# Kernel tuning notes

Measured on AMD Instinct MI355X. Metric: run time of the kernel, lower is better.

## Reference

```python
import jax, jax.numpy as jnp
import numpy as np

N_NODES = 500000
N_EDGES = 600000
N_GRAPHS = 4096
X_DIM = 128
H_DIM = 128
Z_DIM = 64
BN_EPS = 1e-5


def setup_inputs() -> dict:
    key = jax.random.key(0)
    ks = jax.random.split(key, 16)
    inp = {
        'x': jax.random.normal(ks[0], (N_NODES, X_DIM), dtype=jnp.float32),
        'edge_index': jax.random.randint(ks[1], (2, N_EDGES), 0, N_NODES),
        'edge_weights': jax.random.uniform(ks[2], (N_EDGES,), dtype=jnp.float32),
        'y_target': jax.random.uniform(ks[3], (N_GRAPHS, 1), dtype=jnp.float32),
        'batch': jnp.sort(jax.random.randint(ks[4], (N_NODES,), 0, N_GRAPHS)),
        # embedder (single weighted GCN-style layer) params
        'W_self': jax.random.normal(ks[5], (X_DIM, H_DIM), dtype=jnp.float32) / np.sqrt(X_DIM),
        'W_nbr': jax.random.normal(ks[6], (X_DIM, H_DIM), dtype=jnp.float32) / np.sqrt(X_DIM),
        'b_emb': jnp.zeros((H_DIM,), dtype=jnp.float32),
        # encoder_mean head: Linear(h_dim+1, z_dim) + BatchNorm1d(z_dim) + ReLU
        'W_mu': jax.random.normal(ks[7], (H_DIM + 1, Z_DIM), dtype=jnp.float32) / np.sqrt(H_DIM + 1),
        'b_mu': jnp.zeros((Z_DIM,), dtype=jnp.float32),
        'gamma_mu': jnp.ones((Z_DIM,), dtype=jnp.float32),
        'beta_mu': jnp.zeros((Z_DIM,), dtype=jnp.float32),
        # encoder_var head: Linear + BN + ReLU + Sigmoid
        'W_var': jax.random.normal(ks[8], (H_DIM + 1, Z_DIM), dtype=jnp.float32) / np.sqrt(H_DIM + 1),
        'b_var': jnp.zeros((Z_DIM,), dtype=jnp.float32),
        'gamma_var': jnp.ones((Z_DIM,), dtype=jnp.float32),
        'beta_var': jnp.zeros((Z_DIM,), dtype=jnp.float32),
    }
    return inp


def _batchnorm(a, gamma, beta):
    # BatchNorm1d in training mode: per-feature batch stats (biased var)
    mu = jnp.mean(a, axis=0, keepdims=True)
    var = jnp.mean((a - mu) ** 2, axis=0, keepdims=True)
    return (a - mu) * jax.lax.rsqrt(var + BN_EPS) * gamma + beta


def reference(x, edge_index, edge_weights, y_target, batch,
              W_self, W_nbr, b_emb,
              W_mu, b_mu, gamma_mu, beta_mu,
              W_var, b_var, gamma_var, beta_var):
    src, dst = edge_index[0], edge_index[1]
    # embedder.embedding(x, edge_index, edge_weights): weighted neighbor agg + self
    msg = jax.ops.segment_sum(edge_weights[:, None] * x[src], dst, num_segments=N_NODES)
    embed = jax.nn.relu(x @ W_self + msg @ W_nbr + b_emb)  # [N, H]
    # global_mean_pool over graph ids
    sums = jax.ops.segment_sum(embed, batch, num_segments=N_GRAPHS)      # [G, H]
    counts = jax.ops.segment_sum(jnp.ones((embed.shape[0],), embed.dtype), batch,
                                 num_segments=N_GRAPHS)
    graph_emb = sums / jnp.maximum(counts, 1.0)[:, None]
    # concat y_target -> [G, H+1]
    h = jnp.concatenate([graph_emb, y_target], axis=1)
    z_mu = jax.nn.relu(_batchnorm(h @ W_mu + b_mu, gamma_mu, beta_mu))
    z_logvar = jax.nn.sigmoid(jax.nn.relu(_batchnorm(h @ W_var + b_var, gamma_var, beta_var)))
    return (z_mu, z_logvar)
```

## Files before the change

kernel.cpp:

```cpp
#include <hip/hip_runtime.h>
#include <hip/hip_bf16.h>
#include <stdint.h>

#define N_NODES 500000
#define N_EDGES 600000
#define N_GRAPHS 4096
#define XD 128
#define HD 128
#define ZD 64
#define BROWS 64
#define NBUCKETS 7813
#define CAP 120

#define OFF_CURS   0ull
#define OFF_SUMS   8192ull
#define OFF_DEG    532480ull
#define OFF_NINFO  1032704ull
#define OFF_CURSOR 1532928ull
#define OFF_SBUF   2033152ull
#define OFF_AT     3909120ull
#define OFF_STATS  4433408ull
#define OFF_WT     4433664ull
#define OFF_GMEAN  4450048ull
#define OFF_PART   4974336ull
#define OFF_PAY    12974848ull

typedef __attribute__((ext_vector_type(8))) short bf16x8;
typedef __attribute__((ext_vector_type(4))) float f32x4;

__device__ inline uint32_t pk_bf16(float lo, float hi) {
  uint32_t ul = __float_as_uint(lo); ul += 0x7fffu + ((ul >> 16) & 1u);
  uint32_t uh = __float_as_uint(hi); uh += 0x7fffu + ((uh >> 16) & 1u);
  return (ul >> 16) | (uh & 0xffff0000u);
}
__device__ inline float bl16(uint32_t u) { return __uint_as_float(u << 16); }
__device__ inline float bh16(uint32_t u) { return __uint_as_float(u & 0xffff0000u); }

__global__ void wprep_kernel(const float* __restrict__ Wnbr, const float* __restrict__ Wself,
                             uint32_t* __restrict__ wt) {
  const float* __restrict__ W = blockIdx.x ? Wself : Wnbr;
  uint32_t* __restrict__ out = wt + (size_t)blockIdx.x * 8192;
  const int t = threadIdx.x;
  const int n = t >> 1, h = t & 1;
  for (int q = 0; q < 32; ++q) {
    int k2 = h * 32 + q;
    float lo = W[(2 * k2) * HD + n];
    float hi = W[(2 * k2 + 1) * HD + n];
    out[n * 64 + k2] = pk_bf16(lo, hi);
  }
}

__global__ void deg_count(const int* __restrict__ ei, uint32_t* __restrict__ deg) {
  int e = blockIdx.x * blockDim.x + threadIdx.x;
  if (e >= N_EDGES) return;
  atomicAdd(deg + ei[N_EDGES + e], 1u);
}

__global__ void scan_prefix(const uint32_t* __restrict__ deg, uint32_t* __restrict__ nodeinfo,
                            uint32_t* __restrict__ cursor) {
  const int b = blockIdx.x;
  const int lane = threadIdx.x;
  int n = b * BROWS + lane;
  int d = (n < N_NODES) ? (int)deg[n] : 0;
  int s = d;
#pragma unroll
  for (int off = 1; off < 64; off <<= 1) {
    int t = __shfl_up(s, off, 64);
    if (lane >= off) s += t;
  }
  int excl = s - d;
  int st = excl < CAP ? excl : CAP;
  int en = (excl + d) < CAP ? (excl + d) : CAP;
  if (n < N_NODES) {
    nodeinfo[n] = (uint32_t)st | ((uint32_t)en << 8);
    cursor[n] = 0u;
  }
}

__global__ void bucket_fill(const int* __restrict__ ei, const float* __restrict__ ew,
                            const uint32_t* __restrict__ nodeinfo, uint32_t* __restrict__ cursor,
                            int* __restrict__ cur_s, uint2* __restrict__ sbuf,
                            uint32_t* __restrict__ payload) {
  int e = blockIdx.x * blockDim.x + threadIdx.x;
  if (e >= N_EDGES) return;
  int src = ei[e];
  int dst = ei[N_EDGES + e];
  float w = ew[e];
  uint32_t info = nodeinfo[dst];
  int st = (int)(info & 0xffu), en = (int)((info >> 8) & 0xffu);
  int slot = (int)atomicAdd(cursor + dst, 1u);
  int pin = st + slot;
  if (pin >= en) return;
  uint32_t pos = (uint32_t)((dst >> 6) * CAP + pin);
  int bs = src >> 6;
  int ss = atomicAdd(cur_s + bs, 1);
  if (ss < CAP) {
    sbuf[(size_t)bs * CAP + ss] =
        make_uint2(((uint32_t)(src & 63) << 20) | pos, __float_as_uint(w));
  } else {
    uint4 z = make_uint4(0, 0, 0, 0);
    uint4* p = (uint4*)((char*)payload + (size_t)pos * 256);
#pragma unroll
    for (int i = 0; i < 16; ++i) p[i] = z;
  }
}

__launch_bounds__(512, 4)
__global__ void gemm_scatter(const float* __restrict__ x, const uint32_t* __restrict__ wt,
                             const uint2* __restrict__ sbuf, const int* __restrict__ cur_s,
                             uint32_t* __restrict__ payload) {
  __shared__ char lb[33728];
  uint2* srec = (uint2*)(lb + 32768);
  const int b = blockIdx.x;
  const int tid = threadIdx.x;
  const int node0 = b * BROWS;
  const int l = tid & 63, w = tid >> 6;
  const int wm = w >> 2, wn = w & 3;
  const int lr = l & 15, lk = l >> 4;

  {
    const int row = tid >> 3, c8 = tid & 7;
    int m = node0 + row;
    int mc = m < N_NODES ? m : N_NODES - 1;
    const float* xr = x + (size_t)mc * XD + c8 * 16;
    uint32_t p[8];
#pragma unroll
    for (int i = 0; i < 4; ++i) {
      float4 t4 = *(const float4*)(xr + i * 4);
      p[2 * i]     = pk_bf16(t4.x, t4.y);
      p[2 * i + 1] = pk_bf16(t4.z, t4.w);
    }
    char* aw = lb + row * 256;
    const int s0 = c8 * 2;
    *(uint4*)(aw + (((s0)     ^ (row & 7)) << 4)) = make_uint4(p[0], p[1], p[2], p[3]);
    *(uint4*)(aw + (((s0 + 1) ^ (row & 7)) << 4)) = make_uint4(p[4], p[5], p[6], p[7]);
  }
  if (tid < CAP) srec[tid] = sbuf[(size_t)b * CAP + tid];
  __syncthreads();

  f32x4 acc0[2][2];
#pragma unroll
  for (int mf = 0; mf < 2; ++mf) { acc0[mf][0] = (f32x4)0.f; acc0[mf][1] = (f32x4)0.f; }

  {
    const char* wtb = (const char*)wt;
#pragma unroll
    for (int kb = 0; kb < 4; ++kb) {
      int slot = (kb << 2) | lk;
      bf16x8 bf0 = *(const bf16x8*)(wtb + (wn * 32 + lr) * 256 + (kb << 6) + (lk << 4));
      bf16x8 bf1 = *(const bf16x8*)(wtb + (wn * 32 + 16 + lr) * 256 + (kb << 6) + (lk << 4));
#pragma unroll
      for (int mf = 0; mf < 2; ++mf) {
        int r = wm * 32 + mf * 16 + lr;
        bf16x8 a = *(const bf16x8*)(lb + r * 256 + ((slot ^ (r & 7)) << 4));
        acc0[mf][0] = __builtin_amdgcn_mfma_f32_16x16x32_bf16(a, bf0, acc0[mf][0], 0, 0, 0);
        acc0[mf][1] = __builtin_amdgcn_mfma_f32_16x16x32_bf16(a, bf1, acc0[mf][1], 0, 0, 0);
      }
    }
  }
  __syncthreads();

  {
#pragma unroll
    for (int mf = 0; mf < 2; ++mf)
#pragma unroll
      for (int nf = 0; nf < 2; ++nf) {
        int col = wn * 32 + nf * 16 + lr;
#pragma unroll
        for (int r = 0; r < 4; ++r) {
          int row = wm * 32 + mf * 16 + lk * 4 + r;
          uint32_t uv = __float_as_uint(acc0[mf][nf][r]);
          uv += 0x7fffu + ((uv >> 16) & 1u);
          *(unsigned short*)(lb + 16384 + row * 256 + ((col * 2) ^ ((row & 7) << 4))) =
              (unsigned short)(uv >> 16);
        }
      }
  }
  __syncthreads();

  {
    int cnt = cur_s[b]; if (cnt > CAP) cnt = CAP;
    const int eg = tid >> 5;
    const int c = tid & 31;
#pragma unroll
    for (int k = 0; k < 8; ++k) {
      int s = eg + (k << 4);
      if (s < cnt) {
        uint2 rec = srec[s];
        int srcloc = (int)(rec.x >> 20);
        uint32_t pos = rec.x & 0xFFFFFu;
        float wgt = __uint_as_float(rec.y);
        uint2 uv = *(const uint2*)(lb + 16384 + srcloc * 256 + ((c * 8) ^ ((srcloc & 7) << 4)));
        float a0 = bl16(uv.x) * wgt, a1 = bh16(uv.x) * wgt;
        float a2 = bl16(uv.y) * wgt, a3 = bh16(uv.y) * wgt;
        *(uint2*)((char*)payload + (size_t)pos * 256 + c * 8) =
            make_uint2(pk_bf16(a0, a1), pk_bf16(a2, a3));
      }
    }
  }
}

__launch_bounds__(512, 4)
__global__ void accum_pool(const float* __restrict__ x, const uint32_t* __restrict__ payload,
                           const uint32_t* __restrict__ nodeinfo,
                           const uint32_t* __restrict__ wt, const float* __restrict__ bemb,
                           const int* __restrict__ batch,
                           float* __restrict__ partials, float* __restrict__ sums) {
  __shared__ float lds[5200];
  char* astage = (char*)lds;
  float* P = lds + 4096;
  int* span = (int*)(lds + 5120);
  const int b = blockIdx.x;
  const int tid = threadIdx.x;
  const int node0 = b * BROWS;
  const int gfirst = batch[node0];
  const int grp = tid >> 5, c = tid & 31;
  const int l = tid & 63, w = tid >> 6;
  const int wm = w >> 2, wn = w & 3;
  const int lr = l & 15, lk = l >> 4;

  for (int i = tid; i < 1024; i += 512) P[i] = 0.f;
  if (tid < 64) {
    int m = node0 + tid;
    span[tid] = (m < N_NODES) ? (batch[m] - gfirst) : -1;
  }

  {
    const int row = tid >> 3, c8 = tid & 7;
    int m = node0 + row;
    int mc = m < N_NODES ? m : N_NODES - 1;
    const float* xr = x + (size_t)mc * XD + c8 * 16;
    uint32_t p[8];
#pragma unroll
    for (int i = 0; i < 4; ++i) {
      float4 t4 = *(const float4*)(xr + i * 4);
      p[2 * i]     = pk_bf16(t4.x, t4.y);
      p[2 * i + 1] = pk_bf16(t4.z, t4.w);
    }
    char* aw = astage + row * 256;
    const int s0 = c8 * 2;
    *(uint4*)(aw + (((s0)     ^ (row & 7)) << 4)) = make_uint4(p[0], p[1], p[2], p[3]);
    *(uint4*)(aw + (((s0 + 1) ^ (row & 7)) << 4)) = make_uint4(p[4], p[5], p[6], p[7]);
  }
  __syncthreads();

  f32x4 acc1[2][2];
#pragma unroll
  for (int mf = 0; mf < 2; ++mf) { acc1[mf][0] = (f32x4)0.f; acc1[mf][1] = (f32x4)0.f; }
  {
    const char* wtb = (const char*)wt + 32768;
#pragma unroll
    for (int kb = 0; kb < 4; ++kb) {
      int slot = (kb << 2) | lk;
      bf16x8 bf0 = *(const bf16x8*)(wtb + (wn * 32 + lr) * 256 + (kb << 6) + (lk << 4));
      bf16x8 bf1 = *(const bf16x8*)(wtb + (wn * 32 + 16 + lr) * 256 + (kb << 6) + (lk << 4));
#pragma unroll
      for (int mf = 0; mf < 2; ++mf) {
        int r = wm * 32 + mf * 16 + lr;
        bf16x8 a = *(const bf16x8*)(astage + r * 256 + ((slot ^ (r & 7)) << 4));
        acc1[mf][0] = __builtin_amdgcn_mfma_f32_16x16x32_bf16(a, bf0, acc1[mf][0], 0, 0, 0);
        acc1[mf][1] = __builtin_amdgcn_mfma_f32_16x16x32_bf16(a, bf1, acc1[mf][1], 0, 0, 0);
      }
    }
  }
  __syncthreads();

  {
    float be0 = bemb[wn * 32 + lr];
    float be1 = bemb[wn * 32 + 16 + lr];
#pragma unroll
    for (int mf = 0; mf < 2; ++mf)
#pragma unroll
      for (int nf = 0; nf < 2; ++nf) {
        int col = wn * 32 + nf * 16 + lr;
        float be = nf ? be1 : be0;
#pragma unroll
        for (int r = 0; r < 4; ++r) {
          int row = wm * 32 + mf * 16 + lk * 4 + r;
          uint32_t uv = __float_as_uint(acc1[mf][nf][r] + be);
          uv += 0x7fffu + ((uv >> 16) & 1u);
          *(unsigned short*)(astage + row * 256 + ((col * 2) ^ ((row & 7) << 4))) =
              (unsigned short)(uv >> 16);
        }
      }
  }
  __syncthreads();

  {
    float p0 = 0.f, p1 = 0.f, p2 = 0.f, p3 = 0.f;
    int jcur = -1;
#pragma unroll
    for (int rr = 0; rr < 4; ++rr) {
      int row = grp * 4 + rr;
      int n = node0 + row;
      int j = span[row];
      float a0 = 0.f, a1 = 0.f, a2 = 0.f, a3 = 0.f;
      uint32_t info = (n < N_NODES) ? nodeinfo[n] : 0u;
      int st = (int)(info & 0xffu), en = (int)((info >> 8) & 0xffu);
      for (int i = st; i < en; ++i) {
        uint2 pv = *(const uint2*)(payload + ((size_t)b * CAP + i) * 64 + (c << 1));
        a0 += bl16(pv.x); a1 += bh16(pv.x);
        a2 += bl16(pv.y); a3 += bh16(pv.y);
      }
      if (j >= 0) {
        uint2 vv = *(const uint2*)(astage + row * 256 + ((c * 8) ^ ((row & 7) << 4)));
        float z0 = fmaxf(a0 + bl16(vv.x), 0.f);
        float z1 = fmaxf(a1 + bh16(vv.x), 0.f);
        float z2 = fmaxf(a2 + bl16(vv.y), 0.f);
        float z3 = fmaxf(a3 + bh16(vv.y), 0.f);
        if (j != jcur) {
          if (jcur >= 0) {
            if (jcur < 8) {
              atomicAdd(&P[jcur * 128 + 4 * c + 0], p0);
              atomicAdd(&P[jcur * 128 + 4 * c + 1], p1);
              atomicAdd(&P[jcur * 128 + 4 * c + 2], p2);
              atomicAdd(&P[jcur * 128 + 4 * c + 3], p3);
            } else {
              float* sp = sums + (size_t)(gfirst + jcur) * HD + 4 * c;
              atomicAdd(sp + 0, p0); atomicAdd(sp + 1, p1);
              atomicAdd(sp + 2, p2); atomicAdd(sp + 3, p3);
            }
          }
          p0 = p1 = p2 = p3 = 0.f; jcur = j;
        }
        p0 += z0; p1 += z1; p2 += z2; p3 += z3;
      }
    }
    if (jcur >= 0) {
      if (jcur < 8) {
        atomicAdd(&P[jcur * 128 + 4 * c + 0], p0);
        atomicAdd(&P[jcur * 128 + 4 * c + 1], p1);
        atomicAdd(&P[jcur * 128 + 4 * c + 2], p2);
        atomicAdd(&P[jcur * 128 + 4 * c + 3], p3);
      } else {
        float* sp = sums + (size_t)(gfirst + jcur) * HD + 4 * c;
        atomicAdd(sp + 0, p0); atomicAdd(sp + 1, p1);
        atomicAdd(sp + 2, p2); atomicAdd(sp + 3, p3);
      }
    }
  }
  __syncthreads();

  {
    float2 v = *(float2*)&P[tid * 2];
    *(float2*)(partials + (size_t)b * 1024 + tid * 2) = v;
  }
}

__global__ void reduce_mean(const float* __restrict__ partials, const float* __restrict__ sums,
                            const int* __restrict__ batch, float* __restrict__ gmean) {
  const int g = blockIdx.x;
  const int t = threadIdx.x;
  int lo = 0, hi = N_NODES;
  while (lo < hi) { int mid = (lo + hi) >> 1; if (batch[mid] < g) lo = mid + 1; else hi = mid; }
  int s = lo; hi = N_NODES;
  while (lo < hi) { int mid = (lo + hi) >> 1; if (batch[mid] < g + 1) lo = mid + 1; else hi = mid; }
  int e = lo;
  float tot = sums[(size_t)g * HD + t];
  int cnt = e - s;
  if (cnt > 0) {
    int b0 = s >> 6, b1 = (e - 1) >> 6;
    for (int b = b0; b <= b1; ++b) {
      int j = g - batch[b * 64];
      if (j >= 0 && j < 8) tot += partials[(size_t)b * 1024 + j * 128 + t];
    }
  }
  gmean[(size_t)g * HD + t] = tot / fmaxf((float)cnt, 1.f);
}

__global__ void head_kernel(const float* __restrict__ gmean, const float* __restrict__ y,
                            const float* __restrict__ Wmu, const float* __restrict__ bmu,
                            const float* __restrict__ Wvar, const float* __restrict__ bvar,
                            float* __restrict__ aT) {
  __shared__ float hrow[129];
  const int g = blockIdx.x;
  const int t = threadIdx.x;
  hrow[t] = gmean[(size_t)g * HD + t];
  if (t == 0) hrow[128] = y[g];
  __syncthreads();
  const int head = t >> 6, n = t & 63;
  const float* __restrict__ W = head ? Wvar : Wmu;
  float acc = head ? bvar[n] : bmu[n];
  for (int k = 0; k < 129; ++k) acc = fmaf(hrow[k], W[k * ZD + n], acc);
  aT[(size_t)(head * ZD + n) * N_GRAPHS + g] = acc;
}

__global__ void bnstats_kernel(const float* __restrict__ aT, float* __restrict__ stats) {
  const int f = blockIdx.x;
  const float* base = aT + (size_t)f * N_GRAPHS;
  float s = 0.f, ss = 0.f;
  for (int i = threadIdx.x; i < N_GRAPHS; i += 256) { float v = base[i]; s += v; ss += v * v; }
#pragma unroll
  for (int off = 1; off < 64; off <<= 1) { s += __shfl_xor(s, off, 64); ss += __shfl_xor(ss, off, 64); }
  __shared__ float ls[8];
  const int wav = threadIdx.x >> 6, lane = threadIdx.x & 63;
  if (lane == 0) { ls[wav * 2] = s; ls[wav * 2 + 1] = ss; }
  __syncthreads();
  if (threadIdx.x == 0) {
    float S = ls[0] + ls[2] + ls[4] + ls[6];
    float SS = ls[1] + ls[3] + ls[5] + ls[7];
    float mean = S / (float)N_GRAPHS;
    float var = SS / (float)N_GRAPHS - mean * mean;
    stats[f * 2] = mean;
    stats[f * 2 + 1] = rsqrtf(var + 1e-5f);
  }
}

__global__ void bnapply_kernel(const float* __restrict__ aT, const float* __restrict__ stats,
                               const float* __restrict__ gm, const float* __restrict__ btm,
                               const float* __restrict__ gv, const float* __restrict__ btv,
                               float* __restrict__ out) {
  int t = blockIdx.x * blockDim.x + threadIdx.x;
  if (t >= 2 * N_GRAPHS * ZD) return;
  int head = t >> 18;
  int r = t & (N_GRAPHS * ZD - 1);
  int g = r >> 6, n = r & 63;
  int f = (head << 6) | n;
  float v = aT[(size_t)f * N_GRAPHS + g];
  float z = (v - stats[f * 2]) * stats[f * 2 + 1];
  z = z * (head ? gv[n] : gm[n]) + (head ? btv[n] : btm[n]);
  z = fmaxf(z, 0.f);
  if (head) z = 1.f / (1.f + __expf(-z));
  out[t] = z;
}

extern "C" void kernel_launch(void* const* d_in, const int* in_sizes, int n_in,
                              void* d_out, int out_size, void* d_ws, size_t ws_size,
                              hipStream_t stream) {
  const float* x      = (const float*)d_in[0];
  const int*   ei     = (const int*)d_in[1];
  const float* ew     = (const float*)d_in[2];
  const float* y      = (const float*)d_in[3];
  const int*   batch  = (const int*)d_in[4];
  const float* Wself  = (const float*)d_in[5];
  const float* Wnbr   = (const float*)d_in[6];
  const float* bemb   = (const float*)d_in[7];
  const float* Wmu    = (const float*)d_in[8];
  const float* bmu    = (const float*)d_in[9];
  const float* gmu    = (const float*)d_in[10];
  const float* betamu = (const float*)d_in[11];
  const float* Wvar   = (const float*)d_in[12];
  const float* bvar   = (const float*)d_in[13];
  const float* gvar   = (const float*)d_in[14];
  const float* betavar= (const float*)d_in[15];

  float* ws         = (float*)d_ws;
  int*   cur_s      = (int*)(ws + OFF_CURS);
  float* sums       = ws + OFF_SUMS;
  uint32_t* deg     = (uint32_t*)(ws + OFF_DEG);
  uint32_t* ninfo   = (uint32_t*)(ws + OFF_NINFO);
  uint32_t* cursor  = (uint32_t*)(ws + OFF_CURSOR);
  uint2* sbuf       = (uint2*)(ws + OFF_SBUF);
  float* aT         = ws + OFF_AT;
  float* stats      = ws + OFF_STATS;
  uint32_t* wt      = (uint32_t*)(ws + OFF_WT);
  float* gmean      = ws + OFF_GMEAN;
  float* partials   = ws + OFF_PART;
  uint32_t* payload = (uint32_t*)(ws + OFF_PAY);

  hipMemsetAsync(ws, 0, (8192ull + 524288ull + 500224ull) * 4ull, stream);

  wprep_kernel<<<2, 256, 0, stream>>>(Wnbr, Wself, wt);
  deg_count<<<(N_EDGES + 255) / 256, 256, 0, stream>>>(ei, deg);
  scan_prefix<<<NBUCKETS, 64, 0, stream>>>(deg, ninfo, cursor);
  bucket_fill<<<(N_EDGES + 255) / 256, 256, 0, stream>>>(ei, ew, ninfo, cursor,
                                                         cur_s, sbuf, payload);
  gemm_scatter<<<NBUCKETS, 512, 0, stream>>>(x, wt, sbuf, cur_s, payload);
  accum_pool<<<NBUCKETS, 512, 0, stream>>>(x, payload, ninfo, wt, bemb, batch,
                                           partials, sums);
  reduce_mean<<<N_GRAPHS, 128, 0, stream>>>(partials, sums, batch, gmean);
  head_kernel<<<N_GRAPHS, 128, 0, stream>>>(gmean, y, Wmu, bmu, Wvar, bvar, aT);
  bnstats_kernel<<<128, 256, 0, stream>>>(aT, stats);
  bnapply_kernel<<<(2 * N_GRAPHS * ZD + 255) / 256, 256, 0, stream>>>(
      aT, stats, gmu, betamu, gvar, betavar, (float*)d_out);
}
```

Measured before the change: 432.6 us.

## Compute self-GEMM in gemm_scatter, store bf16 V to global, lean pooling kernel

Moves the x@W_self + bias MFMA product out of the pooling kernel and into gemm_scatter, which already has x staged in LDS. The result is written to a new global bf16 buffer, so x is read once instead of twice. The pooling kernel now only gathers the payload and V, uses less LDS, and has a higher occupancy bound. The payload layout also changes from a fixed CAP slot per bucket to a compact prefix-summed layout, built by a new single-block bucket scan. This removes the per-bucket cap on incoming edges, but adds a 128 MB bf16 intermediate round trip and a serial scan launch.

```diff
diff --git a/kernel.cpp b/kernel.cpp
--- a/kernel.cpp
+++ b/kernel.cpp
@@ -17,13 +17,16 @@
 #define OFF_DEG    532480ull
 #define OFF_NINFO  1032704ull
 #define OFF_CURSOR 1532928ull
-#define OFF_SBUF   2033152ull
-#define OFF_AT     3909120ull
-#define OFF_STATS  4433408ull
-#define OFF_WT     4433664ull
-#define OFF_GMEAN  4450048ull
-#define OFF_PART   4974336ull
-#define OFF_PAY    12974848ull
+#define OFF_BTOT   2033152ull
+#define OFF_BBASE  2041344ull
+#define OFF_SBUF   2049536ull
+#define OFF_AT     3925504ull
+#define OFF_STATS  4449792ull
+#define OFF_WT     4450048ull
+#define OFF_GMEAN  4466432ull
+#define OFF_PART   4990720ull
+#define OFF_V      12991232ull
+#define OFF_PAY    44991232ull
 
 typedef __attribute__((ext_vector_type(8))) short bf16x8;
 typedef __attribute__((ext_vector_type(4))) float f32x4;
@@ -57,7 +60,7 @@
 }
 
 __global__ void scan_prefix(const uint32_t* __restrict__ deg, uint32_t* __restrict__ nodeinfo,
-                            uint32_t* __restrict__ cursor) {
+                            uint32_t* __restrict__ cursor, uint32_t* __restrict__ btot) {
   const int b = blockIdx.x;
   const int lane = threadIdx.x;
   int n = b * BROWS + lane;
@@ -69,16 +72,45 @@
     if (lane >= off) s += t;
   }
   int excl = s - d;
-  int st = excl < CAP ? excl : CAP;
-  int en = (excl + d) < CAP ? (excl + d) : CAP;
+  int ex = excl < 255 ? excl : 255;
+  int dc = d < 255 ? d : 255;
   if (n < N_NODES) {
-    nodeinfo[n] = (uint32_t)st | ((uint32_t)en << 8);
+    nodeinfo[n] = (uint32_t)ex | ((uint32_t)dc << 8);
     cursor[n] = 0u;
   }
+  if (lane == 63) btot[b] = (uint32_t)s;
+}
+
+__global__ void scan_buckets(const uint32_t* __restrict__ btot, uint32_t* __restrict__ bbase) {
+  __shared__ uint32_t carry;
+  __shared__ uint32_t wsum[8];
+  if (threadIdx.x == 0) carry = 0u;
+  __syncthreads();
+  for (int off = 0; off < NBUCKETS; off += 512) {
+    int i = off + (int)threadIdx.x;
+    uint32_t d = (i < NBUCKETS) ? btot[i] : 0u;
+    uint32_t s = d;
+#pragma unroll
+    for (int o = 1; o < 64; o <<= 1) {
+      uint32_t t = (uint32_t)__shfl_up((int)s, o, 64);
+      if ((threadIdx.x & 63) >= (unsigned)o) s += t;
+    }
+    int wv = threadIdx.x >> 6, ln = threadIdx.x & 63;
+    if (ln == 63) wsum[wv] = s;
+    __syncthreads();
+    uint32_t woff = 0;
+    for (int k = 0; k < wv; ++k) woff += wsum[k];
+    uint32_t excl = carry + woff + s - d;
+    if (i < NBUCKETS) bbase[i] = excl;
+    __syncthreads();
+    if (threadIdx.x == 511) carry = excl + d;
+    __syncthreads();
+  }
 }
 
 __global__ void bucket_fill(const int* __restrict__ ei, const float* __restrict__ ew,
-                            const uint32_t* __restrict__ nodeinfo, uint32_t* __restrict__ cursor,
+                            const uint32_t* __restrict__ nodeinfo,
+                            const uint32_t* __restrict__ bbase, uint32_t* __restrict__ cursor,
                             int* __restrict__ cur_s, uint2* __restrict__ sbuf,
                             uint32_t* __restrict__ payload) {
   int e = blockIdx.x * blockDim.x + threadIdx.x;
@@ -87,11 +119,10 @@
   int dst = ei[N_EDGES + e];
   float w = ew[e];
   uint32_t info = nodeinfo[dst];
-  int st = (int)(info & 0xffu), en = (int)((info >> 8) & 0xffu);
+  int excl = (int)(info & 0xffu), degc = (int)((info >> 8) & 0xffu);
   int slot = (int)atomicAdd(cursor + dst, 1u);
-  int pin = st + slot;
-  if (pin >= en) return;
-  uint32_t pos = (uint32_t)((dst >> 6) * CAP + pin);
+  if (slot >= degc) return;
+  uint32_t pos = bbase[dst >> 6] + (uint32_t)(excl + slot);
   int bs = src >> 6;
   int ss = atomicAdd(cur_s + bs, 1);
   if (ss < CAP) {
@@ -107,8 +138,9 @@
 
 __launch_bounds__(512, 4)
 __global__ void gemm_scatter(const float* __restrict__ x, const uint32_t* __restrict__ wt,
+                             const float* __restrict__ bemb,
                              const uint2* __restrict__ sbuf, const int* __restrict__ cur_s,
-                             uint32_t* __restrict__ payload) {
+                             uint32_t* __restrict__ payload, uint32_t* __restrict__ Vg) {
   __shared__ char lb[33728];
   uint2* srec = (uint2*)(lb + 32768);
   const int b = blockIdx.x;
@@ -138,9 +170,12 @@
   if (tid < CAP) srec[tid] = sbuf[(size_t)b * CAP + tid];
   __syncthreads();
 
-  f32x4 acc0[2][2];
-#pragma unroll
-  for (int mf = 0; mf < 2; ++mf) { acc0[mf][0] = (f32x4)0.f; acc0[mf][1] = (f32x4)0.f; }
+  f32x4 acc0[2][2], acc1[2][2];
+#pragma unroll
+  for (int mf = 0; mf < 2; ++mf) {
+    acc0[mf][0] = (f32x4)0.f; acc0[mf][1] = (f32x4)0.f;
+    acc1[mf][0] = (f32x4)0.f; acc1[mf][1] = (f32x4)0.f;
+  }
 
   {
     const char* wtb = (const char*)wt;
@@ -158,25 +193,61 @@
       }
     }
   }
-  __syncthreads();
-
-  {
+  {
+    const char* wtb = (const char*)wt + 32768;
+#pragma unroll
+    for (int kb = 0; kb < 4; ++kb) {
+      int slot = (kb << 2) | lk;
+      bf16x8 bf0 = *(const bf16x8*)(wtb + (wn * 32 + lr) * 256 + (kb << 6) + (lk << 4));
+      bf16x8 bf1 = *(const bf16x8*)(wtb + (wn * 32 + 16 + lr) * 256 + (kb << 6) + (lk << 4));
+#pragma unroll
+      for (int mf = 0; mf < 2; ++mf) {
+        int r = wm * 32 + mf * 16 + lr;
+        bf16x8 a = *(const bf16x8*)(lb + r * 256 + ((slot ^ (r & 7)) << 4));
+        acc1[mf][0] = __builtin_amdgcn_mfma_f32_16x16x32_bf16(a, bf0, acc1[mf][0], 0, 0, 0);
+        acc1[mf][1] = __builtin_amdgcn_mfma_f32_16x16x32_bf16(a, bf1, acc1[mf][1], 0, 0, 0);
+      }
+    }
+  }
+  __syncthreads();
+
+  {
+    float be0 = bemb[wn * 32 + lr];
+    float be1 = bemb[wn * 32 + 16 + lr];
 #pragma unroll
     for (int mf = 0; mf < 2; ++mf)
 #pragma unroll
       for (int nf = 0; nf < 2; ++nf) {
         int col = wn * 32 + nf * 16 + lr;
+        float be = nf ? be1 : be0;
 #pragma unroll
         for (int r = 0; r < 4; ++r) {
           int row = wm * 32 + mf * 16 + lk * 4 + r;
-          uint32_t uv = __float_as_uint(acc0[mf][nf][r]);
-          uv += 0x7fffu + ((uv >> 16) & 1u);
+          uint32_t u0 = __float_as_uint(acc0[mf][nf][r]);
+          u0 += 0x7fffu + ((u0 >> 16) & 1u);
           *(unsigned short*)(lb + 16384 + row * 256 + ((col * 2) ^ ((row & 7) << 4))) =
-              (unsigned short)(uv >> 16);
+              (unsigned short)(u0 >> 16);
+          uint32_t u1 = __float_as_uint(acc1[mf][nf][r] + be);
+          u1 += 0x7fffu + ((u1 >> 16) & 1u);
+          *(unsigned short*)(lb + row * 256 + ((col * 2) ^ ((row & 7) << 4))) =
+              (unsigned short)(u1 >> 16);
         }
       }
   }
   __syncthreads();
+
+  {
+    const int row = tid >> 3, seg = tid & 7;
+    const char* cr = lb + row * 256;
+    const int swz = (row & 7) << 4;
+    uint4 v0 = *(const uint4*)(cr + ((seg * 32) ^ swz));
+    uint4 v1 = *(const uint4*)(cr + ((seg * 32 + 16) ^ swz));
+    int m = node0 + row;
+    int mc = m < N_NODES ? m : N_NODES - 1;
+    char* dst = (char*)Vg + (size_t)mc * 256 + seg * 32;
+    *(uint4*)(dst)      = v0;
+    *(uint4*)(dst + 16) = v1;
+  }
 
   {
     int cnt = cur_s[b]; if (cnt > CAP) cnt = CAP;
@@ -200,93 +271,28 @@
   }
 }
 
-__launch_bounds__(512, 4)
-__global__ void accum_pool(const float* __restrict__ x, const uint32_t* __restrict__ payload,
-                           const uint32_t* __restrict__ nodeinfo,
-                           const uint32_t* __restrict__ wt, const float* __restrict__ bemb,
-                           const int* __restrict__ batch,
-                           float* __restrict__ partials, float* __restrict__ sums) {
-  __shared__ float lds[5200];
-  char* astage = (char*)lds;
-  float* P = lds + 4096;
-  int* span = (int*)(lds + 5120);
+__launch_bounds__(512, 8)
+__global__ void pool_lean(const uint32_t* __restrict__ Vg, const uint32_t* __restrict__ payload,
+                          const uint32_t* __restrict__ nodeinfo,
+                          const uint32_t* __restrict__ bbase, const int* __restrict__ batch,
+                          float* __restrict__ partials, float* __restrict__ sums) {
+  __shared__ float P[1024];
+  __shared__ int span[64];
   const int b = blockIdx.x;
   const int tid = threadIdx.x;
   const int node0 = b * BROWS;
   const int gfirst = batch[node0];
   const int grp = tid >> 5, c = tid & 31;
-  const int l = tid & 63, w = tid >> 6;
-  const int wm = w >> 2, wn = w & 3;
-  const int lr = l & 15, lk = l >> 4;
 
   for (int i = tid; i < 1024; i += 512) P[i] = 0.f;
   if (tid < 64) {
     int m = node0 + tid;
     span[tid] = (m < N_NODES) ? (batch[m] - gfirst) : -1;
   }
-
-  {
-    const int row = tid >> 3, c8 = tid & 7;
-    int m = node0 + row;
-    int mc = m < N_NODES ? m : N_NODES - 1;
-    const float* xr = x + (size_t)mc * XD + c8 * 16;
-    uint32_t p[8];
-#pragma unroll
-    for (int i = 0; i < 4; ++i) {
-      float4 t4 = *(const float4*)(xr + i * 4);
-      p[2 * i]     = pk_bf16(t4.x, t4.y);
-      p[2 * i + 1] = pk_bf16(t4.z, t4.w);
-    }
-    char* aw = astage + row * 256;
-    const int s0 = c8 * 2;
-    *(uint4*)(aw + (((s0)     ^ (row & 7)) << 4)) = make_uint4(p[0], p[1], p[2], p[3]);
-    *(uint4*)(aw + (((s0 + 1) ^ (row & 7)) << 4)) = make_uint4(p[4], p[5], p[6], p[7]);
-  }
-  __syncthreads();
-
-  f32x4 acc1[2][2];
-#pragma unroll
-  for (int mf = 0; mf < 2; ++mf) { acc1[mf][0] = (f32x4)0.f; acc1[mf][1] = (f32x4)0.f; }
-  {
-    const char* wtb = (const char*)wt + 32768;
-#pragma unroll
-    for (int kb = 0; kb < 4; ++kb) {
-      int slot = (kb << 2) | lk;
-      bf16x8 bf0 = *(const bf16x8*)(wtb + (wn * 32 + lr) * 256 + (kb << 6) + (lk << 4));
-      bf16x8 bf1 = *(const bf16x8*)(wtb + (wn * 32 + 16 + lr) * 256 + (kb << 6) + (lk << 4));
-#pragma unroll
-      for (int mf = 0; mf < 2; ++mf) {
-        int r = wm * 32 + mf * 16 + lr;
-        bf16x8 a = *(const bf16x8*)(astage + r * 256 + ((slot ^ (r & 7)) << 4));
-        acc1[mf][0] = __builtin_amdgcn_mfma_f32_16x16x32_bf16(a, bf0, acc1[mf][0], 0, 0, 0);
-        acc1[mf][1] = __builtin_amdgcn_mfma_f32_16x16x32_bf16(a, bf1, acc1[mf][1], 0, 0, 0);
-      }
-    }
-  }
-  __syncthreads();
-
-  {
-    float be0 = bemb[wn * 32 + lr];
-    float be1 = bemb[wn * 32 + 16 + lr];
-#pragma unroll
-    for (int mf = 0; mf < 2; ++mf)
-#pragma unroll
-      for (int nf = 0; nf < 2; ++nf) {
-        int col = wn * 32 + nf * 16 + lr;
-        float be = nf ? be1 : be0;
-#pragma unroll
-        for (int r = 0; r < 4; ++r) {
-          int row = wm * 32 + mf * 16 + lk * 4 + r;
-          uint32_t uv = __float_as_uint(acc1[mf][nf][r] + be);
-          uv += 0x7fffu + ((uv >> 16) & 1u);
-          *(unsigned short*)(astage + row * 256 + ((col * 2) ^ ((row & 7) << 4))) =
-              (unsigned short)(uv >> 16);
-        }
-      }
-  }
-  __syncthreads();
-
-  {
+  __syncthreads();
+
+  {
+    const uint32_t base = bbase[b];
     float p0 = 0.f, p1 = 0.f, p2 = 0.f, p3 = 0.f;
     int jcur = -1;
 #pragma unroll
@@ -294,16 +300,17 @@
       int row = grp * 4 + rr;
       int n = node0 + row;
       int j = span[row];
+      uint32_t info = (n < N_NODES) ? nodeinfo[n] : 0u;
+      int excl = (int)(info & 0xffu), dg = (int)((info >> 8) & 0xffu);
+      uint32_t st = base + (uint32_t)excl;
       float a0 = 0.f, a1 = 0.f, a2 = 0.f, a3 = 0.f;
-      uint32_t info = (n < N_NODES) ? nodeinfo[n] : 0u;
-      int st = (int)(info & 0xffu), en = (int)((info >> 8) & 0xffu);
-      for (int i = st; i < en; ++i) {
-        uint2 pv = *(const uint2*)(payload + ((size_t)b * CAP + i) * 64 + (c << 1));
+      for (int i = 0; i < dg; ++i) {
+        uint2 pv = *(const uint2*)(payload + ((size_t)(st + i)) * 64 + (c << 1));
         a0 += bl16(pv.x); a1 += bh16(pv.x);
         a2 += bl16(pv.y); a3 += bh16(pv.y);
       }
       if (j >= 0) {
-        uint2 vv = *(const uint2*)(astage + row * 256 + ((c * 8) ^ ((row & 7) << 4)));
+        uint2 vv = *(const uint2*)(Vg + (size_t)n * 64 + (c << 1));
         float z0 = fmaxf(a0 + bl16(vv.x), 0.f);
         float z1 = fmaxf(a1 + bh16(vv.x), 0.f);
         float z2 = fmaxf(a2 + bl16(vv.y), 0.f);
@@ -450,24 +457,27 @@
   uint32_t* deg     = (uint32_t*)(ws + OFF_DEG);
   uint32_t* ninfo   = (uint32_t*)(ws + OFF_NINFO);
   uint32_t* cursor  = (uint32_t*)(ws + OFF_CURSOR);
+  uint32_t* btot    = (uint32_t*)(ws + OFF_BTOT);
+  uint32_t* bbase   = (uint32_t*)(ws + OFF_BBASE);
   uint2* sbuf       = (uint2*)(ws + OFF_SBUF);
   float* aT         = ws + OFF_AT;
   float* stats      = ws + OFF_STATS;
   uint32_t* wt      = (uint32_t*)(ws + OFF_WT);
   float* gmean      = ws + OFF_GMEAN;
   float* partials   = ws + OFF_PART;
+  uint32_t* Vg      = (uint32_t*)(ws + OFF_V);
   uint32_t* payload = (uint32_t*)(ws + OFF_PAY);
 
   hipMemsetAsync(ws, 0, (8192ull + 524288ull + 500224ull) * 4ull, stream);
 
   wprep_kernel<<<2, 256, 0, stream>>>(Wnbr, Wself, wt);
   deg_count<<<(N_EDGES + 255) / 256, 256, 0, stream>>>(ei, deg);
-  scan_prefix<<<NBUCKETS, 64, 0, stream>>>(deg, ninfo, cursor);
-  bucket_fill<<<(N_EDGES + 255) / 256, 256, 0, stream>>>(ei, ew, ninfo, cursor,
+  scan_prefix<<<NBUCKETS, 64, 0, stream>>>(deg, ninfo, cursor, btot);
+  scan_buckets<<<1, 512, 0, stream>>>(btot, bbase);
+  bucket_fill<<<(N_EDGES + 255) / 256, 256, 0, stream>>>(ei, ew, ninfo, bbase, cursor,
                                                          cur_s, sbuf, payload);
-  gemm_scatter<<<NBUCKETS, 512, 0, stream>>>(x, wt, sbuf, cur_s, payload);
-  accum_pool<<<NBUCKETS, 512, 0, stream>>>(x, payload, ninfo, wt, bemb, batch,
-                                           partials, sums);
+  gemm_scatter<<<NBUCKETS, 512, 0, stream>>>(x, wt, bemb, sbuf, cur_s, payload, Vg);
+  pool_lean<<<NBUCKETS, 512, 0, stream>>>(Vg, payload, ninfo, bbase, batch, partials, sums);
   reduce_mean<<<N_GRAPHS, 128, 0, stream>>>(partials, sums, batch, gmean);
   head_kernel<<<N_GRAPHS, 128, 0, stream>>>(gmean, y, Wmu, bmu, Wvar, bvar, aT);
   bnstats_kernel<<<128, 256, 0, stream>>>(aT, stats);
```

New measurement: 495.4 us. +14.5%, slower.
